# Optimization experiments

Measured on AMD Instinct MI355X. Metric: run time of the kernel, lower is better.

Reference implementation:

```python
import jax, jax.numpy as jnp
import numpy as np

N_NODES = 50000
N_EDGES = 1600000
IN_DIM = 128
HID_DIM = 128
OUT_DIM = 64


def setup_inputs() -> dict:
    key = jax.random.key(0)
    ks = jax.random.split(key, 10)
    n_feat = jax.random.normal(ks[0], (N_NODES, IN_DIM), dtype=jnp.float32)
    edge_weights = jax.random.uniform(ks[1], (N_EDGES, 1), dtype=jnp.float32)
    src = jax.random.randint(ks[2], (N_EDGES,), 0, N_NODES, dtype=jnp.int32)
    dst = jax.random.randint(ks[3], (N_EDGES,), 0, N_NODES, dtype=jnp.int32)
    # Linear(in*2, out) weights, torch layout [out_features, in_features]
    s1 = 1.0 / np.sqrt(2 * IN_DIM)
    s2 = 1.0 / np.sqrt(2 * HID_DIM)
    W1 = jax.random.uniform(ks[4], (HID_DIM, 2 * IN_DIM), jnp.float32, -s1, s1)
    b1 = jax.random.uniform(ks[5], (HID_DIM,), jnp.float32, -s1, s1)
    W2 = jax.random.uniform(ks[6], (HID_DIM, 2 * HID_DIM), jnp.float32, -s2, s2)
    b2 = jax.random.uniform(ks[7], (HID_DIM,), jnp.float32, -s2, s2)
    W3 = jax.random.uniform(ks[8], (OUT_DIM, 2 * HID_DIM), jnp.float32, -s2, s2)
    b3 = jax.random.uniform(ks[9], (OUT_DIM,), jnp.float32, -s2, s2)
    return {"n_feat": n_feat, "edge_weights": edge_weights, "src": src,
            "dst": dst, "W1": W1, "b1": b1, "W2": W2, "b2": b2,
            "W3": W3, "b3": b3}


def reference(n_feat, edge_weights, src, dst, W1, b1, W2, b2, W3, b3):
    N = n_feat.shape[0]
    E = src.shape[0]
    # in-degree for mean aggregation (DGL mean gives 0 for isolated nodes)
    deg = jax.ops.segment_sum(jnp.ones((E,), n_feat.dtype), dst, num_segments=N)
    inv_deg = jnp.where(deg > 0, 1.0 / jnp.maximum(deg, 1.0), 0.0)[:, None]

    def layer(h, W, b):
        m = h[src] * edge_weights                        # [E, d] gather-multiply
        agg = jax.ops.segment_sum(m, dst, num_segments=N) * inv_deg  # mean scatter
        z = jnp.concatenate([agg, h], axis=-1) @ W.T + b
        return jax.nn.relu(z)

    h = layer(n_feat, W1, b1)
    h = layer(h, W2, b2)
    h = layer(h, W3, b3)
    return h
```

## Files before the change

### kernel.cpp

```cpp
#include <hip/hip_runtime.h>

#define NN 50000
#define NE 1600000
#define NPART 196
#define PSZ 256

typedef _Float16 f16;
typedef __attribute__((ext_vector_type(8))) _Float16 f16x8;
typedef __attribute__((ext_vector_type(4))) float f32x4;


__global__ __launch_bounds__(256) void part_count(const int* __restrict__ dst,
                                                  unsigned* __restrict__ pcount, int E) {
    __shared__ unsigned hist[NPART];
    for (int i = threadIdx.x; i < NPART; i += 256) hist[i] = 0;
    __syncthreads();
    for (int e = blockIdx.x * 256 + threadIdx.x; e < E; e += gridDim.x * 256)
        atomicAdd(&hist[((unsigned)dst[e]) >> 8], 1u);
    __syncthreads();
    for (int i = threadIdx.x; i < NPART; i += 256) {
        unsigned c = hist[i];
        if (c) atomicAdd(&pcount[i], c);
    }
}

__global__ void part_scan(const unsigned* __restrict__ pcount,
                          unsigned* __restrict__ poff, unsigned* __restrict__ pcursor) {
    const int t = threadIdx.x;
    const int lane = t & 63, wid = t >> 6;
    __shared__ unsigned wsum[4];
    unsigned v = (t < NPART) ? pcount[t] : 0u;
    unsigned x = v;
    #pragma unroll
    for (int s = 1; s < 64; s <<= 1) {
        unsigned tt = __shfl_up(x, s, 64);
        if (lane >= s) x += tt;
    }
    if (lane == 63) wsum[wid] = x;
    __syncthreads();
    if (t == 0) { unsigned s = 0; for (int k = 0; k < 4; ++k) { unsigned tt = wsum[k]; wsum[k] = s; s += tt; } }
    __syncthreads();
    unsigned excl = x - v + wsum[wid];
    if (t <= NPART) { poff[t] = excl; pcursor[t] = excl; }
}

__global__ __launch_bounds__(512) void bucket_scatter(
    const int* __restrict__ dst, const int* __restrict__ src, const float* __restrict__ ew,
    unsigned* __restrict__ pcursor, unsigned long long* __restrict__ tmp, int E) {
    __shared__ unsigned hist[NPART];
    __shared__ unsigned gbase[NPART];
    const int chunk = blockIdx.x * 8192;
    for (int i = threadIdx.x; i < NPART; i += 512) hist[i] = 0;
    __syncthreads();
    #pragma unroll
    for (int r = 0; r < 16; ++r) {
        int e = chunk + threadIdx.x + r * 512;
        if (e < E) atomicAdd(&hist[((unsigned)dst[e]) >> 8], 1u);
    }
    __syncthreads();
    for (int i = threadIdx.x; i < NPART; i += 512) {
        unsigned c = hist[i];
        gbase[i] = c ? atomicAdd(&pcursor[i], c) : 0u;
        hist[i] = 0;
    }
    __syncthreads();
    #pragma unroll
    for (int r = 0; r < 16; ++r) {
        int e = chunk + threadIdx.x + r * 512;
        if (e < E) {
            unsigned d = (unsigned)dst[e];
            unsigned part = d >> 8;
            unsigned rank = atomicAdd(&hist[part], 1u);
            unsigned long long rec =
                ((unsigned long long)__float_as_uint(ew[e]) << 32)
              | ((unsigned long long)(d & 0xffu) << 16)
              | (unsigned)src[e];
            tmp[gbase[part] + rank] = rec;
        }
    }
}

__global__ __launch_bounds__(256) void part_sort(
    const unsigned long long* __restrict__ tmp, const unsigned* __restrict__ poff,
    unsigned* __restrict__ edges, unsigned* __restrict__ off,
    float* __restrict__ invdeg, int N) {
    __shared__ unsigned hist[PSZ];
    __shared__ unsigned excl[PSZ];
    __shared__ unsigned wsum[4];
    const int b = blockIdx.x;
    const unsigned e0 = poff[b], e1 = poff[b + 1];
    const int t = threadIdx.x;
    hist[t] = 0;
    __syncthreads();
    for (unsigned i = e0 + t; i < e1; i += 256)
        atomicAdd(&hist[(unsigned)(tmp[i] >> 16) & 0xffu], 1u);
    __syncthreads();
    const unsigned v = hist[t];
    const int lane = t & 63, wid = t >> 6;
    unsigned x = v;
    #pragma unroll
    for (int s = 1; s < 64; s <<= 1) {
        unsigned tt = __shfl_up(x, s, 64);
        if (lane >= s) x += tt;
    }
    if (lane == 63) wsum[wid] = x;
    __syncthreads();
    if (t == 0) { unsigned s = 0; for (int k = 0; k < 4; ++k) { unsigned tt = wsum[k]; wsum[k] = s; s += tt; } }
    __syncthreads();
    const unsigned ex = x - v + wsum[wid];
    excl[t] = ex;
    const int node = b * PSZ + t;
    if (node < N) {
        off[node] = e0 + ex;
        invdeg[node] = v ? 1.0f / (float)v : 0.0f;
    }
    if (b == NPART - 1 && t == 0) off[N] = e1;
    hist[t] = 0;
    __syncthreads();
    for (unsigned i = e0 + t; i < e1; i += 256) {
        unsigned long long rec = tmp[i];
        unsigned doff = (unsigned)(rec >> 16) & 0xffu;
        unsigned r = atomicAdd(&hist[doff], 1u);
        union { f16 h; unsigned short u; } cw;
        cw.h = (f16)__uint_as_float((unsigned)(rec >> 32));
        edges[e0 + excl[doff] + r] = ((unsigned)cw.u << 16) | (unsigned)(rec & 0xffffull);
    }
}


__global__ __launch_bounds__(256) void pack_x(const float* __restrict__ in,
                                              f16* __restrict__ out, int n8) {
    int i = blockIdx.x * 256 + threadIdx.x;
    if (i < n8) {
        float4 a = ((const float4*)in)[i * 2];
        float4 b = ((const float4*)in)[i * 2 + 1];
        f16x8 h;
        h[0] = (f16)a.x; h[1] = (f16)a.y; h[2] = (f16)a.z; h[3] = (f16)a.w;
        h[4] = (f16)b.x; h[5] = (f16)b.y; h[6] = (f16)b.z; h[7] = (f16)b.w;
        ((f16x8*)out)[i] = h;
    }
}


template <int OUTH>
__global__ __launch_bounds__(256) void gemm_mfma(
    const f16* __restrict__ X, const float* __restrict__ W,
    const float* __restrict__ bias,
    f16* __restrict__ Pout,
    f16* __restrict__ Qout,
    int N)
{
    const int tile = blockIdx.x * 64;
    const int colbase = blockIdx.y * 64;
    const int t = threadIdx.x;
    const int lane = t & 63;
    const int wv = t >> 6;

    __shared__ f16 Xs[64 * 128];
    __shared__ f16 Ws[64 * 128];

    #pragma unroll
    for (int i = 0; i < 4; ++i) {
        int row = i * 16 + (t >> 4);
        int chunk = t & 15;
        int v = tile + row;
        uint4 val = make_uint4(0u, 0u, 0u, 0u);
        if (v < N) val = ((const uint4*)(X + (size_t)v * 128))[chunk];
        ((uint4*)Xs)[row * 16 + (chunk ^ (row & 7))] = val;
    }
    const int isq = (colbase >= OUTH);
    #pragma unroll
    for (int i = 0; i < 4; ++i) {
        int row = i * 16 + (t >> 4);
        int chunk = t & 15;
        int c = colbase + row;
        const float* wsrc = W + (size_t)(isq ? c - OUTH : c) * 256 + (isq ? 128 : 0) + chunk * 8;
        float4 wa = *(const float4*)wsrc;
        float4 wb = *(const float4*)(wsrc + 4);
        f16x8 wh;
        wh[0] = (f16)wa.x; wh[1] = (f16)wa.y; wh[2] = (f16)wa.z; wh[3] = (f16)wa.w;
        wh[4] = (f16)wb.x; wh[5] = (f16)wb.y; wh[6] = (f16)wb.z; wh[7] = (f16)wb.w;
        ((f16x8*)Ws)[row * 16 + (chunk ^ (row & 7))] = wh;
    }
    __syncthreads();

    const int lr = lane & 15;
    const int kg = lane >> 4;
    f16x8 afrag[4];
    #pragma unroll
    for (int kb = 0; kb < 4; ++kb) {
        int row = wv * 16 + lr;
        afrag[kb] = ((const f16x8*)Xs)[row * 16 + ((kb * 4 + kg) ^ (row & 7))];
    }
    f32x4 acc[4];
    #pragma unroll
    for (int nt = 0; nt < 4; ++nt)
        #pragma unroll
        for (int j = 0; j < 4; ++j) acc[nt][j] = 0.0f;

    #pragma unroll
    for (int nt = 0; nt < 4; ++nt) {
        int col = nt * 16 + lr;
        #pragma unroll
        for (int kb = 0; kb < 4; ++kb) {
            f16x8 bfrag = ((const f16x8*)Ws)[col * 16 + ((kb * 4 + kg) ^ (col & 7))];
            acc[nt] = __builtin_amdgcn_mfma_f32_16x16x32_f16(afrag[kb], bfrag, acc[nt], 0, 0, 0);
        }
    }

    #pragma unroll
    for (int nt = 0; nt < 4; ++nt) {
        int c = colbase + nt * 16 + lr;
        #pragma unroll
        for (int j = 0; j < 4; ++j) {
            int v = tile + wv * 16 + kg * 4 + j;
            if (v >= N) continue;
            if (!isq) {
                Pout[(size_t)v * OUTH + c] = (f16)acc[nt][j];
            } else {
                int qc = c - OUTH;
                Qout[(size_t)v * OUTH + qc] = (f16)(acc[nt][j] + bias[qc]);
            }
        }
    }
}


#define AGG_STEP(REC) {                                                         \
    unsigned srcv = (REC) & 0xffffu;                                            \
    float wvv; { union { unsigned short u; f16 h; } cw;                         \
                 cw.u = (unsigned short)((REC) >> 16); wvv = (float)cw.h; }     \
    const uint4 r = *(const uint4*)(P + (size_t)srcv * DIM + lr * 8);           \
    union { uint4 u; f16 h[8]; } c_; c_.u = r;                                  \
    a[0] = fmaf((float)c_.h[0], wvv, a[0]);                                     \
    a[1] = fmaf((float)c_.h[1], wvv, a[1]);                                     \
    a[2] = fmaf((float)c_.h[2], wvv, a[2]);                                     \
    a[3] = fmaf((float)c_.h[3], wvv, a[3]);                                     \
    a[4] = fmaf((float)c_.h[4], wvv, a[4]);                                     \
    a[5] = fmaf((float)c_.h[5], wvv, a[5]);                                     \
    a[6] = fmaf((float)c_.h[6], wvv, a[6]);                                     \
    a[7] = fmaf((float)c_.h[7], wvv, a[7]); }

template <int LPR, bool F16OUT>
__global__ __launch_bounds__(256) void agg_fused(
    const f16* __restrict__ P,
    const f16* __restrict__ Qh,
    const unsigned* __restrict__ edges,
    const unsigned* __restrict__ off, const float* __restrict__ invdeg,
    void* __restrict__ outv)
{
    constexpr int DIM = LPR * 8;
    constexpr int G   = 64 / LPR;
    const int node = blockIdx.x * 4 + (threadIdx.x >> 6);
    const int lane = threadIdx.x & 63;
    const int g    = lane / LPR;
    const int lr   = lane % LPR;
    const unsigned s0 = off[node], s1 = off[node + 1];
    const unsigned deg = s1 - s0;
    const float inv = invdeg[node];

    float a[8];
    #pragma unroll
    for (int i = 0; i < 8; ++i) a[i] = 0.f;

    const unsigned* __restrict__ ep = edges + s0 + g;
    const unsigned nfull = deg / G;
    #pragma unroll 8
    for (unsigned it = 0; it < nfull; ++it) {
        unsigned rec = ep[(size_t)it * G];
        AGG_STEP(rec);
    }
    if ((unsigned)g < (deg - nfull * G)) {
        unsigned rec = ep[(size_t)nfull * G];
        AGG_STEP(rec);
    }

    #pragma unroll
    for (int i = 0; i < 8; ++i) {
        a[i] += __shfl_xor(a[i], 32, 64);
        a[i] += __shfl_xor(a[i], 16, 64);
        if (LPR == 8) a[i] += __shfl_xor(a[i], 8, 64);
    }

    if (lane < LPR) {
        f16x8 q = *(const f16x8*)(Qh + (size_t)node * DIM + lr * 8);
        float o[8];
        #pragma unroll
        for (int i = 0; i < 8; ++i)
            o[i] = fmaxf(fmaf(a[i], inv, (float)q[i]), 0.f);
        if (F16OUT) {
            f16x8 h;
            #pragma unroll
            for (int i = 0; i < 8; ++i) h[i] = (f16)o[i];
            *(f16x8*)((f16*)outv + (size_t)node * DIM + lr * 8) = h;
        } else {
            float* out = (float*)outv;
            *(float4*)&out[(size_t)node * DIM + lr * 8]     = make_float4(o[0], o[1], o[2], o[3]);
            *(float4*)&out[(size_t)node * DIM + lr * 8 + 4] = make_float4(o[4], o[5], o[6], o[7]);
        }
    }
}


extern "C" void kernel_launch(void* const* d_in, const int* in_sizes, int n_in,
                              void* d_out, int out_size, void* d_ws, size_t ws_size,
                              hipStream_t stream) {
    const float* n_feat = (const float*)d_in[0];
    const float* ew     = (const float*)d_in[1];
    const int*   src    = (const int*)d_in[2];
    const int*   dst    = (const int*)d_in[3];
    const float* W1 = (const float*)d_in[4];
    const float* b1 = (const float*)d_in[5];
    const float* W2 = (const float*)d_in[6];
    const float* b2 = (const float*)d_in[7];
    const float* W3 = (const float*)d_in[8];
    const float* b3 = (const float*)d_in[9];

    const int N = NN, E = NE;

    uint8_t* w = (uint8_t*)d_ws;
    size_t o = 0;
    auto carve = [&](size_t bytes) { uint8_t* p = w + o; o += (bytes + 255) & ~(size_t)255; return p; };
    unsigned* pcount  = (unsigned*)carve((size_t)NPART * 4);
    unsigned* poff    = (unsigned*)carve((size_t)(NPART + 1) * 4);
    unsigned* pcursor = (unsigned*)carve((size_t)(NPART + 1) * 4);
    unsigned* off     = (unsigned*)carve((size_t)(N + 1) * 4);
    float*    invdeg  = (float*)   carve((size_t)N * 4);
    unsigned* edges   = (unsigned*)carve((size_t)E * 4);
    f16*      Xf      = (f16*)     carve((size_t)N * 128 * 2);
    f16*      H       = (f16*)     carve((size_t)N * 128 * 2);
    f16*      P       = (f16*)     carve((size_t)N * 128 * 2);
    size_t qbytes = (size_t)N * 128 * 2;
    size_t tbytes = (size_t)E * 8;
    f16*      Qh      = (f16*)     carve(qbytes > tbytes ? qbytes : tbytes);
    unsigned long long* tmp = (unsigned long long*)Qh;

    float* OUT = (float*)d_out;

    hipMemsetAsync(pcount, 0, (size_t)NPART * 4, stream);
    part_count<<<392, 256, 0, stream>>>(dst, pcount, E);
    part_scan<<<1, 256, 0, stream>>>(pcount, poff, pcursor);
    bucket_scatter<<<(E + 8191) / 8192, 512, 0, stream>>>(dst, src, ew, pcursor, tmp, E);
    part_sort<<<NPART, 256, 0, stream>>>(tmp, poff, edges, off, invdeg, N);

    const int gx = (N + 63) / 64;
    const int ga = N / 4;

    pack_x<<<(N * 16 + 255) / 256, 256, 0, stream>>>(n_feat, Xf, N * 16);
    gemm_mfma<128><<<dim3(gx, 4), 256, 0, stream>>>(Xf, W1, b1, P, Qh, N);
    agg_fused<16, true><<<ga, 256, 0, stream>>>(P, Qh, edges, off, invdeg, H);

    gemm_mfma<128><<<dim3(gx, 4), 256, 0, stream>>>(H, W2, b2, P, Qh, N);
    agg_fused<16, true><<<ga, 256, 0, stream>>>(P, Qh, edges, off, invdeg, H);

    gemm_mfma<64><<<dim3(gx, 2), 256, 0, stream>>>(H, W3, b3, P, Qh, N);
    agg_fused<8, false><<<ga, 256, 0, stream>>>(P, Qh, edges, off, invdeg, OUT);
}
```

Before: 273.2 us.

## Fuse fp32-to-fp16 packing into GEMM, finer partitions, nontemporal agg loads/stores

Removes the separate pack_x kernel by having the first GEMM read the fp32 features directly and convert them to fp16 while loading tiles. It also halves the partition size for the edge bucketing (391 partitions of 128 nodes) so part_sort runs more, smaller blocks, and switches edge/Q loads and output stores in the aggregation kernel to nontemporal hints. The tradeoff is that the first GEMM reads fp32 data four times (once per column block), that more partitions mean more global atomics in the scatter, and that nontemporal hints may reduce L2 reuse of the Q reads.

```diff
diff --git a/kernel.cpp b/kernel.cpp
--- a/kernel.cpp
+++ b/kernel.cpp
@@ -2,12 +2,13 @@
 
 #define NN 50000
 #define NE 1600000
-#define NPART 196
-#define PSZ 256
+#define NPART 391
+#define PSZ 128
 
 typedef _Float16 f16;
 typedef __attribute__((ext_vector_type(8))) _Float16 f16x8;
 typedef __attribute__((ext_vector_type(4))) float f32x4;
+typedef __attribute__((ext_vector_type(4))) unsigned u32x4;
 
 
 __global__ __launch_bounds__(256) void part_count(const int* __restrict__ dst,
@@ -16,7 +17,7 @@
     for (int i = threadIdx.x; i < NPART; i += 256) hist[i] = 0;
     __syncthreads();
     for (int e = blockIdx.x * 256 + threadIdx.x; e < E; e += gridDim.x * 256)
-        atomicAdd(&hist[((unsigned)dst[e]) >> 8], 1u);
+        atomicAdd(&hist[((unsigned)dst[e]) >> 7], 1u);
     __syncthreads();
     for (int i = threadIdx.x; i < NPART; i += 256) {
         unsigned c = hist[i];
@@ -24,11 +25,12 @@
     }
 }
 
-__global__ void part_scan(const unsigned* __restrict__ pcount,
-                          unsigned* __restrict__ poff, unsigned* __restrict__ pcursor) {
+__global__ __launch_bounds__(512) void part_scan(const unsigned* __restrict__ pcount,
+                                                 unsigned* __restrict__ poff,
+                                                 unsigned* __restrict__ pcursor) {
     const int t = threadIdx.x;
     const int lane = t & 63, wid = t >> 6;
-    __shared__ unsigned wsum[4];
+    __shared__ unsigned wsum[8];
     unsigned v = (t < NPART) ? pcount[t] : 0u;
     unsigned x = v;
     #pragma unroll
@@ -38,7 +40,7 @@
     }
     if (lane == 63) wsum[wid] = x;
     __syncthreads();
-    if (t == 0) { unsigned s = 0; for (int k = 0; k < 4; ++k) { unsigned tt = wsum[k]; wsum[k] = s; s += tt; } }
+    if (t == 0) { unsigned s = 0; for (int k = 0; k < 8; ++k) { unsigned tt = wsum[k]; wsum[k] = s; s += tt; } }
     __syncthreads();
     unsigned excl = x - v + wsum[wid];
     if (t <= NPART) { poff[t] = excl; pcursor[t] = excl; }
@@ -55,7 +57,7 @@
     #pragma unroll
     for (int r = 0; r < 16; ++r) {
         int e = chunk + threadIdx.x + r * 512;
-        if (e < E) atomicAdd(&hist[((unsigned)dst[e]) >> 8], 1u);
+        if (e < E) atomicAdd(&hist[((unsigned)dst[e]) >> 7], 1u);
     }
     __syncthreads();
     for (int i = threadIdx.x; i < NPART; i += 512) {
@@ -69,31 +71,31 @@
         int e = chunk + threadIdx.x + r * 512;
         if (e < E) {
             unsigned d = (unsigned)dst[e];
-            unsigned part = d >> 8;
+            unsigned part = d >> 7;
             unsigned rank = atomicAdd(&hist[part], 1u);
             unsigned long long rec =
                 ((unsigned long long)__float_as_uint(ew[e]) << 32)
-              | ((unsigned long long)(d & 0xffu) << 16)
+              | ((unsigned long long)(d & 0x7fu) << 16)
               | (unsigned)src[e];
             tmp[gbase[part] + rank] = rec;
         }
     }
 }
 
-__global__ __launch_bounds__(256) void part_sort(
+__global__ __launch_bounds__(PSZ) void part_sort(
     const unsigned long long* __restrict__ tmp, const unsigned* __restrict__ poff,
     unsigned* __restrict__ edges, unsigned* __restrict__ off,
     float* __restrict__ invdeg, int N) {
     __shared__ unsigned hist[PSZ];
     __shared__ unsigned excl[PSZ];
-    __shared__ unsigned wsum[4];
+    __shared__ unsigned wsum[2];
     const int b = blockIdx.x;
     const unsigned e0 = poff[b], e1 = poff[b + 1];
     const int t = threadIdx.x;
     hist[t] = 0;
     __syncthreads();
-    for (unsigned i = e0 + t; i < e1; i += 256)
-        atomicAdd(&hist[(unsigned)(tmp[i] >> 16) & 0xffu], 1u);
+    for (unsigned i = e0 + t; i < e1; i += PSZ)
+        atomicAdd(&hist[(unsigned)(tmp[i] >> 16) & 0x7fu], 1u);
     __syncthreads();
     const unsigned v = hist[t];
     const int lane = t & 63, wid = t >> 6;
@@ -105,7 +107,7 @@
     }
     if (lane == 63) wsum[wid] = x;
     __syncthreads();
-    if (t == 0) { unsigned s = 0; for (int k = 0; k < 4; ++k) { unsigned tt = wsum[k]; wsum[k] = s; s += tt; } }
+    if (t == 0) { unsigned s = wsum[0]; wsum[0] = 0; wsum[1] = s; }
     __syncthreads();
     const unsigned ex = x - v + wsum[wid];
     excl[t] = ex;
@@ -117,9 +119,9 @@
     if (b == NPART - 1 && t == 0) off[N] = e1;
     hist[t] = 0;
     __syncthreads();
-    for (unsigned i = e0 + t; i < e1; i += 256) {
+    for (unsigned i = e0 + t; i < e1; i += PSZ) {
         unsigned long long rec = tmp[i];
-        unsigned doff = (unsigned)(rec >> 16) & 0xffu;
+        unsigned doff = (unsigned)(rec >> 16) & 0x7fu;
         unsigned r = atomicAdd(&hist[doff], 1u);
         union { f16 h; unsigned short u; } cw;
         cw.h = (f16)__uint_as_float((unsigned)(rec >> 32));
@@ -128,23 +130,9 @@
 }
 
 
-__global__ __launch_bounds__(256) void pack_x(const float* __restrict__ in,
-                                              f16* __restrict__ out, int n8) {
-    int i = blockIdx.x * 256 + threadIdx.x;
-    if (i < n8) {
-        float4 a = ((const float4*)in)[i * 2];
-        float4 b = ((const float4*)in)[i * 2 + 1];
-        f16x8 h;
-        h[0] = (f16)a.x; h[1] = (f16)a.y; h[2] = (f16)a.z; h[3] = (f16)a.w;
-        h[4] = (f16)b.x; h[5] = (f16)b.y; h[6] = (f16)b.z; h[7] = (f16)b.w;
-        ((f16x8*)out)[i] = h;
-    }
-}
-
-
-template <int OUTH>
+template <int OUTH, bool XF32>
 __global__ __launch_bounds__(256) void gemm_mfma(
-    const f16* __restrict__ X, const float* __restrict__ W,
+    const void* __restrict__ Xv, const float* __restrict__ W,
     const float* __restrict__ bias,
     f16* __restrict__ Pout,
     f16* __restrict__ Qout,
@@ -164,9 +152,19 @@
         int row = i * 16 + (t >> 4);
         int chunk = t & 15;
         int v = tile + row;
-        uint4 val = make_uint4(0u, 0u, 0u, 0u);
-        if (v < N) val = ((const uint4*)(X + (size_t)v * 128))[chunk];
-        ((uint4*)Xs)[row * 16 + (chunk ^ (row & 7))] = val;
+        f16x8 hv = {0, 0, 0, 0, 0, 0, 0, 0};
+        if (v < N) {
+            if (XF32) {
+                const float* xp = (const float*)Xv + (size_t)v * 128 + chunk * 8;
+                float4 a = *(const float4*)xp;
+                float4 b = *(const float4*)(xp + 4);
+                hv[0] = (f16)a.x; hv[1] = (f16)a.y; hv[2] = (f16)a.z; hv[3] = (f16)a.w;
+                hv[4] = (f16)b.x; hv[5] = (f16)b.y; hv[6] = (f16)b.z; hv[7] = (f16)b.w;
+            } else {
+                hv = ((const f16x8*)((const f16*)Xv + (size_t)v * 128))[chunk];
+            }
+        }
+        ((f16x8*)Xs)[row * 16 + (chunk ^ (row & 7))] = hv;
     }
     const int isq = (colbase >= OUTH);
     #pragma unroll
@@ -267,11 +265,11 @@
     const unsigned nfull = deg / G;
     #pragma unroll 8
     for (unsigned it = 0; it < nfull; ++it) {
-        unsigned rec = ep[(size_t)it * G];
+        unsigned rec = __builtin_nontemporal_load(ep + (size_t)it * G);
         AGG_STEP(rec);
     }
     if ((unsigned)g < (deg - nfull * G)) {
-        unsigned rec = ep[(size_t)nfull * G];
+        unsigned rec = __builtin_nontemporal_load(ep + (size_t)nfull * G);
         AGG_STEP(rec);
     }
 
@@ -283,20 +281,23 @@
     }
 
     if (lane < LPR) {
-        f16x8 q = *(const f16x8*)(Qh + (size_t)node * DIM + lr * 8);
+        u32x4 qu = __builtin_nontemporal_load((const u32x4*)(Qh + (size_t)node * DIM + lr * 8));
+        union { u32x4 u; f16 h[8]; } qc; qc.u = qu;
         float o[8];
         #pragma unroll
         for (int i = 0; i < 8; ++i)
-            o[i] = fmaxf(fmaf(a[i], inv, (float)q[i]), 0.f);
+            o[i] = fmaxf(fmaf(a[i], inv, (float)qc.h[i]), 0.f);
         if (F16OUT) {
-            f16x8 h;
+            union { u32x4 u; f16 h[8]; } hc;
             #pragma unroll
-            for (int i = 0; i < 8; ++i) h[i] = (f16)o[i];
-            *(f16x8*)((f16*)outv + (size_t)node * DIM + lr * 8) = h;
+            for (int i = 0; i < 8; ++i) hc.h[i] = (f16)o[i];
+            __builtin_nontemporal_store(hc.u, (u32x4*)((f16*)outv + (size_t)node * DIM + lr * 8));
         } else {
             float* out = (float*)outv;
-            *(float4*)&out[(size_t)node * DIM + lr * 8]     = make_float4(o[0], o[1], o[2], o[3]);
-            *(float4*)&out[(size_t)node * DIM + lr * 8 + 4] = make_float4(o[4], o[5], o[6], o[7]);
+            f32x4 o0 = {o[0], o[1], o[2], o[3]};
+            f32x4 o1 = {o[4], o[5], o[6], o[7]};
+            __builtin_nontemporal_store(o0, (f32x4*)&out[(size_t)node * DIM + lr * 8]);
+            __builtin_nontemporal_store(o1, (f32x4*)&out[(size_t)node * DIM + lr * 8 + 4]);
         }
     }
 }
@@ -321,13 +322,12 @@
     uint8_t* w = (uint8_t*)d_ws;
     size_t o = 0;
     auto carve = [&](size_t bytes) { uint8_t* p = w + o; o += (bytes + 255) & ~(size_t)255; return p; };
-    unsigned* pcount  = (unsigned*)carve((size_t)NPART * 4);
+    unsigned* pcount  = (unsigned*)carve((size_t)(NPART + 1) * 4);
     unsigned* poff    = (unsigned*)carve((size_t)(NPART + 1) * 4);
     unsigned* pcursor = (unsigned*)carve((size_t)(NPART + 1) * 4);
     unsigned* off     = (unsigned*)carve((size_t)(N + 1) * 4);
     float*    invdeg  = (float*)   carve((size_t)N * 4);
     unsigned* edges   = (unsigned*)carve((size_t)E * 4);
-    f16*      Xf      = (f16*)     carve((size_t)N * 128 * 2);
     f16*      H       = (f16*)     carve((size_t)N * 128 * 2);
     f16*      P       = (f16*)     carve((size_t)N * 128 * 2);
     size_t qbytes = (size_t)N * 128 * 2;
@@ -337,22 +337,21 @@
 
     float* OUT = (float*)d_out;
 
-    hipMemsetAsync(pcount, 0, (size_t)NPART * 4, stream);
+    hipMemsetAsync(pcount, 0, (size_t)(NPART + 1) * 4, stream);
     part_count<<<392, 256, 0, stream>>>(dst, pcount, E);
-    part_scan<<<1, 256, 0, stream>>>(pcount, poff, pcursor);
+    part_scan<<<1, 512, 0, stream>>>(pcount, poff, pcursor);
     bucket_scatter<<<(E + 8191) / 8192, 512, 0, stream>>>(dst, src, ew, pcursor, tmp, E);
-    part_sort<<<NPART, 256, 0, stream>>>(tmp, poff, edges, off, invdeg, N);
+    part_sort<<<NPART, PSZ, 0, stream>>>(tmp, poff, edges, off, invdeg, N);
 
     const int gx = (N + 63) / 64;
     const int ga = N / 4;
 
-    pack_x<<<(N * 16 + 255) / 256, 256, 0, stream>>>(n_feat, Xf, N * 16);
-    gemm_mfma<128><<<dim3(gx, 4), 256, 0, stream>>>(Xf, W1, b1, P, Qh, N);
+    gemm_mfma<128, true><<<dim3(gx, 4), 256, 0, stream>>>(n_feat, W1, b1, P, Qh, N);
     agg_fused<16, true><<<ga, 256, 0, stream>>>(P, Qh, edges, off, invdeg, H);
 
-    gemm_mfma<128><<<dim3(gx, 4), 256, 0, stream>>>(H, W2, b2, P, Qh, N);
+    gemm_mfma<128, false><<<dim3(gx, 4), 256, 0, stream>>>(H, W2, b2, P, Qh, N);
     agg_fused<16, true><<<ga, 256, 0, stream>>>(P, Qh, edges, off, invdeg, H);
 
-    gemm_mfma<64><<<dim3(gx, 2), 256, 0, stream>>>(H, W3, b3, P, Qh, N);
+    gemm_mfma<64, false><<<dim3(gx, 2), 256, 0, stream>>>(H, W3, b3, P, Qh, N);
     agg_fused<8, false><<<ga, 256, 0, stream>>>(P, Qh, edges, off, invdeg, OUT);
 }
```

After: 300.4 us. 1.1x slower.
